# Kernel tuning notes

Measured on AMD Instinct MI355X. Metric: run time of the kernel, lower is better.

Reference implementation:

```python
import jax, jax.numpy as jnp
import numpy as np

B, N, F, C, K = 4, 8192, 128, 64, 16


def setup_inputs() -> dict:
    key = jax.random.key(0)
    ks = jax.random.split(key, 24)
    s = 0.05
    rn = lambda k, shape: (jax.random.normal(k, shape, jnp.float32) * s)
    return {
        "features": jax.random.normal(ks[0], (B, N, F), jnp.float32),
        "positions": jax.random.normal(ks[1], (B, N, 3), jnp.float32),
        "batch": jnp.repeat(jnp.arange(B, dtype=jnp.int32), N),
        "num_neighbors": K,
        # linear encoder (F -> C)
        "W_enc": rn(ks[2], (F, C)), "b_enc": jnp.zeros((C,), jnp.float32),
        # point-transformer q/k/v projections (C -> C)
        "Wq": rn(ks[3], (C, C)), "bq": jnp.zeros((C,), jnp.float32),
        "Wk": rn(ks[4], (C, C)), "bk": jnp.zeros((C,), jnp.float32),
        "Wv": rn(ks[5], (C, C)), "bv": jnp.zeros((C,), jnp.float32),
        # positional encoding MLP: 3 -> C -> C (ReLU)
        "Wp1": rn(ks[6], (3, C)), "bp1": jnp.zeros((C,), jnp.float32),
        "Wp2": rn(ks[7], (C, C)), "bp2": jnp.zeros((C,), jnp.float32),
        # attention MLP gamma: C -> C -> C (ReLU)
        "Wa1": rn(ks[8], (C, C)), "ba1": jnp.zeros((C,), jnp.float32),
        "Wa2": rn(ks[9], (C, C)), "ba2": jnp.zeros((C,), jnp.float32),
        # linear decoder (C -> F)
        "W_dec": rn(ks[10], (C, F)), "b_dec": jnp.zeros((F,), jnp.float32),
    }


def reference(features, positions, batch, num_neighbors,
              W_enc, b_enc, Wq, bq, Wk, bk, Wv, bv,
              Wp1, bp1, Wp2, bp2, Wa1, ba1, Wa2, ba2, W_dec, b_dec):
    # linear encode: [B,N,F] -> [B,N,C]
    x = features @ W_enc + b_enc
    q = x @ Wq + bq
    k = x @ Wk + bk
    v = x @ Wv + bv

    def per_cloud(pos, qi, ki, vi):
        # kNN via pairwise squared distances (self included, dist 0)
        sq = jnp.sum(pos * pos, axis=-1)                      # [N]
        d2 = sq[:, None] + sq[None, :] - 2.0 * (pos @ pos.T)  # [N,N]
        idx = jax.lax.top_k(-d2, num_neighbors)[1]            # [N,K]
        kj = ki[idx]                                          # [N,K,C] gather
        vj = vi[idx]                                          # [N,K,C]
        rel = pos[:, None, :] - pos[idx]                      # [N,K,3]
        # positional encoding delta = MLP(p_i - p_j)
        delta = jax.nn.relu(rel @ Wp1 + bp1) @ Wp2 + bp2      # [N,K,C]
        # vector attention: gamma(q_i - k_j + delta), softmax over K neighbors
        a = qi[:, None, :] - kj + delta
        a = jax.nn.relu(a @ Wa1 + ba1) @ Wa2 + ba2
        w = jax.nn.softmax(a, axis=1)                         # [N,K,C]
        return jnp.sum(w * (vj + delta), axis=1)              # [N,C]

    y = jax.vmap(per_cloud)(positions, q, k, v)               # [B,N,C]
    out = y @ W_dec + b_dec + features                        # decode + residual
    return (out, positions, batch)
```

## Files before the change

### kernel.cpp

```cpp
#include <hip/hip_runtime.h>
#include <hip/hip_bf16.h>

#define NPTS 32768
#define NPC  8192
#define KNN  16
#define CH   64
#define FDIM 128
#define NCELLS 4096
#define EMPTYKEY 0x7F7FFFFFu

typedef __bf16 bf16;
typedef __bf16 bf16x2 __attribute__((ext_vector_type(2)));
typedef __bf16 bf16x8 __attribute__((ext_vector_type(8)));
typedef float  f32x4  __attribute__((ext_vector_type(4)));

__device__ __forceinline__ unsigned spread4(unsigned v) {
    return (v & 1u) | ((v & 2u) << 2) | ((v & 4u) << 4) | ((v & 8u) << 6);
}

__global__ __launch_bounds__(1024) void k_sort(
    const float* __restrict__ pos, int* __restrict__ perm,
    int* __restrict__ invperm, float* __restrict__ posS)
{
    __shared__ unsigned hist[NCELLS];
    __shared__ unsigned short cellOf[NPC];
    __shared__ unsigned partial[1024];
    int cloud = blockIdx.x;
    int t = threadIdx.x;
    int cb = cloud * NPC;
    const float* pc = pos + (size_t)cb * 3;

    for (int i = t; i < NCELLS; i += 1024) hist[i] = 0;
    __syncthreads();

    for (int i = t; i < NPC; i += 1024) {
        float x = pc[i*3+0], y = pc[i*3+1], z = pc[i*3+2];
        int xi = (int)((x + 4.f) * 2.f); xi = xi < 0 ? 0 : (xi > 15 ? 15 : xi);
        int yi = (int)((y + 4.f) * 2.f); yi = yi < 0 ? 0 : (yi > 15 ? 15 : yi);
        int zi = (int)((z + 4.f) * 2.f); zi = zi < 0 ? 0 : (zi > 15 ? 15 : zi);
        unsigned m = (spread4((unsigned)xi) << 2) | (spread4((unsigned)yi) << 1) | spread4((unsigned)zi);
        cellOf[i] = (unsigned short)m;
        atomicAdd(&hist[m], 1u);
    }
    __syncthreads();

    unsigned s0 = hist[4*t+0], s1 = hist[4*t+1], s2 = hist[4*t+2], s3 = hist[4*t+3];
    unsigned tot = s0 + s1 + s2 + s3;
    partial[t] = tot;
    __syncthreads();
    for (int off = 1; off < 1024; off <<= 1) {
        unsigned v = (t >= off) ? partial[t - off] : 0u;
        __syncthreads();
        partial[t] += v;
        __syncthreads();
    }
    unsigned base = (t > 0) ? partial[t-1] : 0u;
    hist[4*t+0] = base;
    hist[4*t+1] = base + s0;
    hist[4*t+2] = base + s0 + s1;
    hist[4*t+3] = base + s0 + s1 + s2;
    __syncthreads();

    for (int i = t; i < NPC; i += 1024) {
        unsigned c = cellOf[i];
        unsigned s = atomicAdd(&hist[c], 1u);
        perm[cb + (int)s] = cb + i;
        invperm[cb + i] = cb + (int)s;
        posS[(size_t)(cb + (int)s)*3 + 0] = pc[i*3+0];
        posS[(size_t)(cb + (int)s)*3 + 1] = pc[i*3+1];
        posS[(size_t)(cb + (int)s)*3 + 2] = pc[i*3+2];
    }
}

__global__ __launch_bounds__(256) void k_encode(
    const float* __restrict__ feat, const int* __restrict__ perm,
    const float* __restrict__ Wenc, const float* __restrict__ benc,
    const float* __restrict__ Wq, const float* __restrict__ bq,
    const float* __restrict__ Wk, const float* __restrict__ bk,
    const float* __restrict__ Wv, const float* __restrict__ bv,
    bf16* __restrict__ qo, bf16* __restrict__ kvo)
{
    __shared__ float xs[4][CH];
    int t = threadIdx.x;
    int c = t & 63, pl = t >> 6;
    size_t pt = (size_t)blockIdx.x * 4 + pl;
    size_t orig = (size_t)perm[pt];
    const float* fr = feat + orig * FDIM;
    float acc = benc[c];
#pragma unroll 8
    for (int f4 = 0; f4 < 32; ++f4) {
        float4 fv = *reinterpret_cast<const float4*>(fr + f4 * 4);
        acc += fv.x * Wenc[(f4*4+0)*CH + c];
        acc += fv.y * Wenc[(f4*4+1)*CH + c];
        acc += fv.z * Wenc[(f4*4+2)*CH + c];
        acc += fv.w * Wenc[(f4*4+3)*CH + c];
    }
    xs[pl][c] = acc;
    __syncthreads();
    float aq = bq[c], ak = bk[c], av = bv[c];
#pragma unroll 4
    for (int m = 0; m < CH; ++m) {
        float xm = xs[pl][m];
        aq += xm * Wq[m*CH + c];
        ak += xm * Wk[m*CH + c];
        av += xm * Wv[m*CH + c];
    }
    qo[pt*CH + c] = (bf16)aq;
    bf16x2 kv2; kv2[0] = (bf16)ak; kv2[1] = (bf16)av;
    *reinterpret_cast<bf16x2*>(&kvo[pt*2*CH + 2*c]) = kv2;
}

__global__ __launch_bounds__(256, 4) void k_knn(
    const float* __restrict__ pos, unsigned* __restrict__ wsK)
{
    __shared__ float4 sp[1024];
    __shared__ unsigned sbuf[256 * 17];

    int t = threadIdx.x;
    int blk = blockIdx.x;
    int slice = blk & 7;
    int qg = (blk >> 3) & 31;
    int cloud = blk >> 8;
    const float* pc = pos + (size_t)cloud * NPC * 3;
    int jbase = slice << 10;

    {
        const float4* src = reinterpret_cast<const float4*>(pc + (size_t)jbase * 3);
        float4 a = src[t*3+0], b1 = src[t*3+1], c1 = src[t*3+2];
        sp[t*4+0] = make_float4(a.x,  a.y,  a.z,  0.f);
        sp[t*4+1] = make_float4(a.w,  b1.x, b1.y, 0.f);
        sp[t*4+2] = make_float4(b1.z, b1.w, c1.x, 0.f);
        sp[t*4+3] = make_float4(c1.y, c1.z, c1.w, 0.f);
    }
    __syncthreads();

    int qi = (qg << 8) + t;
    float myx = pc[qi*3+0], myy = pc[qi*3+1], myz = pc[qi*3+2];

    unsigned arr[16];
#pragma unroll
    for (int r = 0; r < 16; ++r) arr[r] = EMPTYKEY;
    float thrf = __uint_as_float(EMPTYKEY & 0xFFFFE000u);
    int cnt = 0;
    int base = t * 17;

    for (int g = 0; g < 1024; g += 4) {
        float d2v[4];
#pragma unroll
        for (int u = 0; u < 4; ++u) {
            float4 p = sp[g + u];
            float dx = myx - p.x, dy = myy - p.y, dz = myz - p.z;
            d2v[u] = dx*dx + dy*dy + dz*dz;
        }
        float m4 = fminf(fminf(d2v[0], d2v[1]), fminf(d2v[2], d2v[3]));
        if (__any(m4 <= thrf)) {
#pragma unroll
            for (int u = 0; u < 4; ++u) {
                if (d2v[u] <= thrf) {
                    sbuf[base + cnt] = (__float_as_uint(d2v[u]) & 0xFFFFE000u)
                                       | (unsigned)(jbase + g + u);
                    ++cnt;
                }
            }
            if (__any(cnt >= 13)) {
#pragma unroll
                for (int b = 0; b < 16; ++b) {
                    unsigned key = (b < cnt) ? sbuf[base + b] : EMPTYKEY;
                    if (key < arr[15]) {
#pragma unroll
                        for (int r = 0; r < 16; ++r) {
                            unsigned lo = min(key, arr[r]);
                            unsigned hi = max(key, arr[r]);
                            arr[r] = lo; key = hi;
                        }
                    }
                }
                cnt = 0;
                thrf = __uint_as_float(arr[15] & 0xFFFFE000u);
            }
        }
    }
#pragma unroll
    for (int b = 0; b < 16; ++b) {
        unsigned key = (b < cnt) ? sbuf[base + b] : EMPTYKEY;
        if (key < arr[15]) {
#pragma unroll
            for (int r = 0; r < 16; ++r) {
                unsigned lo = min(key, arr[r]);
                unsigned hi = max(key, arr[r]);
                arr[r] = lo; key = hi;
            }
        }
    }
    size_t gq = (size_t)cloud * NPC + qi;
#pragma unroll
    for (int r = 0; r < 16; ++r) wsK[(size_t)(slice*16 + r)*NPTS + gq] = arr[r];
}

__global__ __launch_bounds__(64) void k_merge(
    const unsigned* __restrict__ wsK, const int* __restrict__ invperm,
    int* __restrict__ idxout,
    const float* __restrict__ Wp2, const float* __restrict__ Wa1,
    const float* __restrict__ Wa2, bf16* __restrict__ wpk)
{
    __shared__ unsigned kk[64][137];
    int t = threadIdx.x;
    size_t q = (size_t)blockIdx.x * 64 + t;
    int cb = (int)((q >> 13) << 13);
#pragma unroll
    for (int l = 0; l < 8; ++l) {
#pragma unroll
        for (int r = 0; r < 16; ++r)
            kk[t][l*17 + r] = wsK[(size_t)(l*16 + r)*NPTS + q];
        kk[t][l*17 + 16] = 0xFFFFFFFFu;
    }

    int sq = invperm[q];
    unsigned h0=0,h1=0,h2=0,h3=0,h4=0,h5=0,h6=0,h7=0;
    int* o = idxout + (size_t)sq * KNN;
    for (int r = 0; r < KNN; ++r) {
        unsigned best = 0xFFFFFFFFu; int bl = 0; unsigned k;
        k = kk[t][0*17 + h0]; if (k < best) { best = k; bl = 0; }
        k = kk[t][1*17 + h1]; if (k < best) { best = k; bl = 1; }
        k = kk[t][2*17 + h2]; if (k < best) { best = k; bl = 2; }
        k = kk[t][3*17 + h3]; if (k < best) { best = k; bl = 3; }
        k = kk[t][4*17 + h4]; if (k < best) { best = k; bl = 4; }
        k = kk[t][5*17 + h5]; if (k < best) { best = k; bl = 5; }
        k = kk[t][6*17 + h6]; if (k < best) { best = k; bl = 6; }
        k = kk[t][7*17 + h7]; if (k < best) { best = k; bl = 7; }
        o[r] = invperm[cb + (int)(best & 0x1FFFu)] - cb;
        h0 += (bl == 0); h1 += (bl == 1); h2 += (bl == 2); h3 += (bl == 3);
        h4 += (bl == 4); h5 += (bl == 5); h6 += (bl == 6); h7 += (bl == 7);
    }

    if (blockIdx.x == 0) {
        int lane = t;
        int mlane = lane & 15, kgrp = lane >> 4;
        const float* Ws[3] = {Wp2, Wa1, Wa2};
        bf16x8* ow = reinterpret_cast<bf16x8*>(wpk);
        for (int gmm = 0; gmm < 3; ++gmm) {
#pragma unroll
            for (int nt = 0; nt < 4; ++nt) {
#pragma unroll
                for (int kt = 0; kt < 2; ++kt) {
                    bf16x8 v;
#pragma unroll
                    for (int j = 0; j < 8; ++j)
                        v[j] = (bf16)Ws[gmm][(kt*32 + kgrp*8 + j)*CH + nt*16 + mlane];
                    ow[(gmm*8 + nt*2 + kt)*64 + lane] = v;
                }
            }
        }
    }
}

__device__ __forceinline__ void wave_gemm(
    const bf16* At, f32x4 (&acc)[4][4], const bf16x8* __restrict__ wpk,
    int w, int lane)
{
    int kgrp = lane >> 4;
    bf16x8 wf[4][2];
#pragma unroll
    for (int nt = 0; nt < 4; ++nt)
#pragma unroll
        for (int kt = 0; kt < 2; ++kt)
            wf[nt][kt] = wpk[(nt*2 + kt)*64 + lane];
#pragma unroll
    for (int mt = 0; mt < 4; ++mt) {
        int row = w*64 + mt*16 + (lane & 15);
        const bf16* rb = At + row*CH;
        int sw = row & 7;
        bf16x8 a0 = *reinterpret_cast<const bf16x8*>(rb + ((kgrp     ^ sw) * 8));
        bf16x8 a1 = *reinterpret_cast<const bf16x8*>(rb + (((4+kgrp) ^ sw) * 8));
#pragma unroll
        for (int nt = 0; nt < 4; ++nt) {
            acc[mt][nt] = __builtin_amdgcn_mfma_f32_16x16x32_bf16(a0, wf[nt][0], acc[mt][nt], 0, 0, 0);
            acc[mt][nt] = __builtin_amdgcn_mfma_f32_16x16x32_bf16(a1, wf[nt][1], acc[mt][nt], 0, 0, 0);
        }
    }
}

__global__ __launch_bounds__(128, 3) void k_attn(
    const float* __restrict__ pos, const int* __restrict__ nidx,
    const bf16* __restrict__ qg, const bf16* __restrict__ kvg,
    const float* __restrict__ Wp1, const float* __restrict__ bp1,
    const float* __restrict__ bp2, const float* __restrict__ ba1,
    const float* __restrict__ ba2, const bf16* __restrict__ wpkg,
    float* __restrict__ yout)
{
    __shared__ bf16 At[128 * CH];

    int t = threadIdx.x;
    int w = t >> 6, lane = t & 63;
    int mlane = lane & 15, kgrp = lane >> 4;
    int blk0 = blockIdx.x;
    int blk = ((blk0 & 7) << 9) | (blk0 >> 3);
    size_t p0 = (size_t)blk * 8;
    size_t cbase = (p0 >> 13) << 13;
    const bf16x2* kv2 = reinterpret_cast<const bf16x2*>(kvg);
    const bf16x8* wpk = reinterpret_cast<const bf16x8*>(wpkg);

    {
        int p = t >> 4, j = t & 15;
        size_t gp = p0 + p;
        int nbr = nidx[gp*KNN + j];
        size_t gn = cbase + (size_t)nbr;
        float rx = pos[gp*3+0] - pos[gn*3+0];
        float ry = pos[gp*3+1] - pos[gn*3+1];
        float rz = pos[gp*3+2] - pos[gn*3+2];
        float h[CH];
#pragma unroll
        for (int c4 = 0; c4 < 16; ++c4) {
            float4 w0 = *reinterpret_cast<const float4*>(Wp1 + 0*CH + c4*4);
            float4 w1 = *reinterpret_cast<const float4*>(Wp1 + 1*CH + c4*4);
            float4 w2 = *reinterpret_cast<const float4*>(Wp1 + 2*CH + c4*4);
            float4 bb = *reinterpret_cast<const float4*>(bp1 + c4*4);
            h[c4*4+0] = fmaxf(rx*w0.x + ry*w1.x + rz*w2.x + bb.x, 0.f);
            h[c4*4+1] = fmaxf(rx*w0.y + ry*w1.y + rz*w2.y + bb.y, 0.f);
            h[c4*4+2] = fmaxf(rx*w0.z + ry*w1.z + rz*w2.z + bb.z, 0.f);
            h[c4*4+3] = fmaxf(rx*w0.w + ry*w1.w + rz*w2.w + bb.w, 0.f);
        }
#pragma unroll
        for (int ch = 0; ch < 8; ++ch) {
            bf16x8 v;
#pragma unroll
            for (int e = 0; e < 8; ++e) v[e] = (bf16)h[ch*8 + e];
            *reinterpret_cast<bf16x8*>(&At[t*CH + (ch ^ (t & 7)) * 8]) = v;
        }
    }

    f32x4 acc[4][4];

#pragma unroll
    for (int nt = 0; nt < 4; ++nt) {
        float b = bp2[nt*16 + mlane];
#pragma unroll
        for (int mt = 0; mt < 4; ++mt) { acc[mt][nt][0]=b; acc[mt][nt][1]=b; acc[mt][nt][2]=b; acc[mt][nt][3]=b; }
    }
    wave_gemm(At, acc, wpk, w, lane);

    bf16x2 vdp[4][4][2];
#pragma unroll
    for (int mt = 0; mt < 4; ++mt) {
        size_t gp = p0 + (size_t)(w*4 + mt);
        int nb[4];
#pragma unroll
        for (int reg = 0; reg < 4; ++reg)
            nb[reg] = nidx[gp*KNN + kgrp*4 + reg];
#pragma unroll
        for (int nt = 0; nt < 4; ++nt) {
            int c = nt*16 + mlane;
            float qv = (float)qg[gp*CH + c];
            float vdf[4];
#pragma unroll
            for (int reg = 0; reg < 4; ++reg) {
                float dlt = acc[mt][nt][reg];
                size_t gr = cbase + (size_t)nb[reg];
                bf16x2 kvp = kv2[gr*CH + c];
                float kvf = (float)kvp[0];
                float vv  = (float)kvp[1];
                int row = w*64 + mt*16 + kgrp*4 + reg;
                int off = row*CH + (((c >> 3) ^ (row & 7)) * 8) + (c & 7);
                At[off] = (bf16)(qv - kvf + dlt);
                vdf[reg] = vv + dlt;
            }
            bf16x2 lo2; lo2[0] = (bf16)vdf[0]; lo2[1] = (bf16)vdf[1];
            bf16x2 hi2; hi2[0] = (bf16)vdf[2]; hi2[1] = (bf16)vdf[3];
            vdp[mt][nt][0] = lo2;
            vdp[mt][nt][1] = hi2;
        }
    }

#pragma unroll
    for (int nt = 0; nt < 4; ++nt) {
        float b = ba1[nt*16 + mlane];
#pragma unroll
        for (int mt = 0; mt < 4; ++mt) { acc[mt][nt][0]=b; acc[mt][nt][1]=b; acc[mt][nt][2]=b; acc[mt][nt][3]=b; }
    }
    wave_gemm(At, acc, wpk + 512, w, lane);
#pragma unroll
    for (int mt = 0; mt < 4; ++mt) {
#pragma unroll
        for (int nt = 0; nt < 4; ++nt) {
            int c = nt*16 + mlane;
#pragma unroll
            for (int reg = 0; reg < 4; ++reg) {
                int row = w*64 + mt*16 + kgrp*4 + reg;
                int off = row*CH + (((c >> 3) ^ (row & 7)) * 8) + (c & 7);
                At[off] = (bf16)fmaxf(acc[mt][nt][reg], 0.f);
            }
        }
    }

#pragma unroll
    for (int nt = 0; nt < 4; ++nt) {
        float b = ba2[nt*16 + mlane];
#pragma unroll
        for (int mt = 0; mt < 4; ++mt) { acc[mt][nt][0]=b; acc[mt][nt][1]=b; acc[mt][nt][2]=b; acc[mt][nt][3]=b; }
    }
    wave_gemm(At, acc, wpk + 1024, w, lane);

#pragma unroll
    for (int mt = 0; mt < 4; ++mt) {
        size_t gp = p0 + (size_t)(w*4 + mt);
#pragma unroll
        for (int nt = 0; nt < 4; ++nt) {
            int c = nt*16 + mlane;
            float m = fmaxf(fmaxf(acc[mt][nt][0], acc[mt][nt][1]),
                            fmaxf(acc[mt][nt][2], acc[mt][nt][3]));
            m = fmaxf(m, __shfl_xor(m, 16));
            m = fmaxf(m, __shfl_xor(m, 32));
            float e[4], s = 0.f;
#pragma unroll
            for (int reg = 0; reg < 4; ++reg) { e[reg] = __expf(acc[mt][nt][reg] - m); s += e[reg]; }
            s += __shfl_xor(s, 16);
            s += __shfl_xor(s, 32);
            float num = 0.f;
            num += e[0] * (float)vdp[mt][nt][0][0];
            num += e[1] * (float)vdp[mt][nt][0][1];
            num += e[2] * (float)vdp[mt][nt][1][0];
            num += e[3] * (float)vdp[mt][nt][1][1];
            num += __shfl_xor(num, 16);
            num += __shfl_xor(num, 32);
            if (kgrp == 0) yout[gp*CH + c] = num / s;
        }
    }
}

__global__ __launch_bounds__(256) void k_decode(
    const float* __restrict__ y, const int* __restrict__ invperm,
    const float* __restrict__ Wd, const float* __restrict__ bd,
    const float* __restrict__ feat, const float* __restrict__ pos,
    const int* __restrict__ batch, float* __restrict__ out)
{
    int t = threadIdx.x;
    int f = t & 127, pl = t >> 7;
    size_t pt = (size_t)blockIdx.x * 2 + pl;
    const float* yr = y + (size_t)invperm[pt]*CH;
    float acc = bd[f] + feat[pt*FDIM + f];
#pragma unroll
    for (int c4 = 0; c4 < 16; ++c4) {
        float4 yv = *reinterpret_cast<const float4*>(yr + c4*4);
        acc += yv.x * Wd[(c4*4+0)*FDIM + f];
        acc += yv.y * Wd[(c4*4+1)*FDIM + f];
        acc += yv.z * Wd[(c4*4+2)*FDIM + f];
        acc += yv.w * Wd[(c4*4+3)*FDIM + f];
    }
    out[pt*FDIM + f] = acc;

    int i = blockIdx.x * 256 + t;
    if (i < NPTS*3) out[(size_t)NPTS*FDIM + i] = pos[i];
    if (i < NPTS)   out[(size_t)NPTS*FDIM + NPTS*3 + i] = (float)batch[i];
}

extern "C" void kernel_launch(void* const* d_in, const int* in_sizes, int n_in,
                              void* d_out, int out_size, void* d_ws, size_t ws_size,
                              hipStream_t stream)
{
    const float* feat  = (const float*)d_in[0];
    const float* pos   = (const float*)d_in[1];
    const int*   batch = (const int*)d_in[2];
    const float* Wenc  = (const float*)d_in[4];
    const float* benc  = (const float*)d_in[5];
    const float* Wq = (const float*)d_in[6];   const float* bq = (const float*)d_in[7];
    const float* Wk = (const float*)d_in[8];   const float* bk = (const float*)d_in[9];
    const float* Wv = (const float*)d_in[10];  const float* bv = (const float*)d_in[11];
    const float* Wp1= (const float*)d_in[12];  const float* bp1= (const float*)d_in[13];
    const float* Wp2= (const float*)d_in[14];  const float* bp2= (const float*)d_in[15];
    const float* Wa1= (const float*)d_in[16];  const float* ba1= (const float*)d_in[17];
    const float* Wa2= (const float*)d_in[18];  const float* ba2= (const float*)d_in[19];
    const float* Wd = (const float*)d_in[20];  const float* bd = (const float*)d_in[21];
    float* out = (float*)d_out;

    char* W = (char*)d_ws;
    int*      idx = (int*)W;
    unsigned* wsK = (unsigned*)(W + (size_t)NPTS*KNN*4);
    bf16* qb  = (bf16*)wsK;
    bf16* kvb = qb + (size_t)NPTS*CH;
    float* yb = (float*)(W + (size_t)NPTS*KNN*4 + (size_t)NPTS*KNN*8*4);
    bf16*  wpk = (bf16*)(yb + (size_t)NPTS*CH);
    int*   perm    = (int*)((char*)wpk + 32768);
    int*   invperm = perm + NPTS;
    float* posS    = (float*)(invperm + NPTS);

    k_sort<<<4, 1024, 0, stream>>>(pos, perm, invperm, posS);
    k_knn<<<1024, 256, 0, stream>>>(pos, wsK);
    k_merge<<<NPTS/64, 64, 0, stream>>>(wsK, invperm, idx, Wp2, Wa1, Wa2, wpk);

    k_encode<<<NPTS/4, 256, 0, stream>>>(feat, perm, Wenc, benc, Wq, bq, Wk, bk, Wv, bv, qb, kvb);

    k_attn<<<NPTS/8, 128, 0, stream>>>(posS, idx, qb, kvb,
                                       Wp1, bp1, bp2, ba1, ba2, wpk, yb);

    k_decode<<<NPTS/2, 256, 0, stream>>>(yb, invperm, Wd, bd, feat, pos, batch, out);
}
```

Measured before the change: 476.4 us.

## Compute kNN distances with bf16 split-precision MFMA instead of scalar FMA

The brute-force kNN distance loop now runs on the matrix cores via mfma_f32_16x16x32_bf16. Coordinates are split into hi/lo bf16 parts to keep roughly fp32 accuracy, and a norm term is folded in. The work is repartitioned so each lane handles one query against a quarter of each 16-candidate tile, with candidates staged into LDS in chunks. Occupancy is lowered to 3 blocks per CU to fit the larger shared tile. The bf16 split could misorder near-tied neighbors, and per-lane candidate insertion stays scalar.

```diff
diff --git a/kernel.cpp b/kernel.cpp
--- a/kernel.cpp
+++ b/kernel.cpp
@@ -110,32 +110,34 @@
     *reinterpret_cast<bf16x2*>(&kvo[pt*2*CH + 2*c]) = kv2;
 }
 
-__global__ __launch_bounds__(256, 4) void k_knn(
+__global__ __launch_bounds__(256, 3) void k_knn(
     const float* __restrict__ pos, unsigned* __restrict__ wsK)
 {
-    __shared__ float4 sp[1024];
+    __shared__ bf16 Atile[1024 * 16];
     __shared__ unsigned sbuf[256 * 17];
 
     int t = threadIdx.x;
     int blk = blockIdx.x;
-    int slice = blk & 7;
-    int qg = (blk >> 3) & 31;
     int cloud = blk >> 8;
+    int half  = blk & 1;
+    int qg    = (blk >> 1) & 127;
     const float* pc = pos + (size_t)cloud * NPC * 3;
-    int jbase = slice << 10;
-
-    {
-        const float4* src = reinterpret_cast<const float4*>(pc + (size_t)jbase * 3);
-        float4 a = src[t*3+0], b1 = src[t*3+1], c1 = src[t*3+2];
-        sp[t*4+0] = make_float4(a.x,  a.y,  a.z,  0.f);
-        sp[t*4+1] = make_float4(a.w,  b1.x, b1.y, 0.f);
-        sp[t*4+2] = make_float4(b1.z, b1.w, c1.x, 0.f);
-        sp[t*4+3] = make_float4(c1.y, c1.z, c1.w, 0.f);
-    }
-    __syncthreads();
-
-    int qi = (qg << 8) + t;
-    float myx = pc[qi*3+0], myy = pc[qi*3+1], myz = pc[qi*3+2];
+
+    int w = t >> 6, lane = t & 63;
+    int col = lane & 15, kgrp = lane >> 4;
+
+    int q = qg*64 + w*16 + col;
+    float qx = pc[q*3+0], qy = pc[q*3+1], qz = pc[q*3+2];
+    float qq = fmaf(qx, qx, fmaf(qy, qy, qz*qz));
+    float nx = -qx, ny = -qy, nz = -qz;
+    bf16 nhx = (bf16)nx; bf16 nlx = (bf16)(nx - (float)nhx);
+    bf16 nhy = (bf16)ny; bf16 nly = (bf16)(ny - (float)nhy);
+    bf16 nhz = (bf16)nz; bf16 nlz = (bf16)(nz - (float)nhz);
+    bf16 Z = (bf16)0.f, ONE = (bf16)1.f;
+    bf16x8 bfrag;
+    if (kgrp == 0)      bfrag = (bf16x8){nhx,nhy,nhz,nhx,nhy,nhz,nlx,nly};
+    else if (kgrp == 1) bfrag = (bf16x8){nlz,ONE,ONE,nlx,nly,nlz,Z,Z};
+    else                bfrag = (bf16x8){Z,Z,Z,Z,Z,Z,Z,Z};
 
     unsigned arr[16];
 #pragma unroll
@@ -144,21 +146,38 @@
     int cnt = 0;
     int base = t * 17;
 
-    for (int g = 0; g < 1024; g += 4) {
-        float d2v[4];
-#pragma unroll
-        for (int u = 0; u < 4; ++u) {
-            float4 p = sp[g + u];
-            float dx = myx - p.x, dy = myy - p.y, dz = myz - p.z;
-            d2v[u] = dx*dx + dy*dy + dz*dz;
-        }
-        float m4 = fminf(fminf(d2v[0], d2v[1]), fminf(d2v[2], d2v[3]));
-        if (__any(m4 <= thrf)) {
-#pragma unroll
-            for (int u = 0; u < 4; ++u) {
-                if (d2v[u] <= thrf) {
-                    sbuf[base + cnt] = (__float_as_uint(d2v[u]) & 0xFFFFE000u)
-                                       | (unsigned)(jbase + g + u);
+    for (int chunk = 0; chunk < 4; ++chunk) {
+        __syncthreads();
+#pragma unroll
+        for (int i = 0; i < 4; ++i) {
+            int lc = i*256 + t;
+            int cand = half*4096 + chunk*1024 + lc;
+            float px = pc[cand*3+0], py = pc[cand*3+1], pz = pc[cand*3+2];
+            float wv = 0.5f * fmaf(px, px, fmaf(py, py, pz*pz));
+            bf16 phx = (bf16)px; bf16 plx = (bf16)(px - (float)phx);
+            bf16 phy = (bf16)py; bf16 ply = (bf16)(py - (float)phy);
+            bf16 phz = (bf16)pz; bf16 plz = (bf16)(pz - (float)phz);
+            bf16 wh  = (bf16)wv; bf16 wl  = (bf16)(wv - (float)wh);
+            bf16x8 lo = (bf16x8){phx,phy,phz,plx,ply,plz,phx,phy};
+            bf16x8 hi = (bf16x8){phz,wh,wl,plx,ply,plz,Z,Z};
+            int off = (lc >> 4)*256 + (lc & 15)*16;
+            *reinterpret_cast<bf16x8*>(&Atile[off])     = lo;
+            *reinterpret_cast<bf16x8*>(&Atile[off + 8]) = hi;
+        }
+        __syncthreads();
+
+        int cb0 = half*4096 + chunk*1024 + kgrp*4;
+        for (int tile = 0; tile < 64; ++tile) {
+            int aoff = tile*256 + col*16 + (kgrp & 1)*8;
+            bf16x8 a = *reinterpret_cast<const bf16x8*>(&Atile[aoff]);
+            f32x4 acc = {0.f, 0.f, 0.f, 0.f};
+            acc = __builtin_amdgcn_mfma_f32_16x16x32_bf16(a, bfrag, acc, 0, 0, 0);
+#pragma unroll
+            for (int reg = 0; reg < 4; ++reg) {
+                float d2 = fmaxf(fmaf(2.f, acc[reg], qq), 0.f);
+                if (d2 <= thrf) {
+                    sbuf[base + cnt] = (__float_as_uint(d2) & 0xFFFFE000u)
+                                       | (unsigned)(cb0 + tile*16 + reg);
                     ++cnt;
                 }
             }
@@ -169,9 +188,9 @@
                     if (key < arr[15]) {
 #pragma unroll
                         for (int r = 0; r < 16; ++r) {
-                            unsigned lo = min(key, arr[r]);
-                            unsigned hi = max(key, arr[r]);
-                            arr[r] = lo; key = hi;
+                            unsigned klo = min(key, arr[r]);
+                            unsigned khi = max(key, arr[r]);
+                            arr[r] = klo; key = khi;
                         }
                     }
                 }
@@ -186,15 +205,16 @@
         if (key < arr[15]) {
 #pragma unroll
             for (int r = 0; r < 16; ++r) {
-                unsigned lo = min(key, arr[r]);
-                unsigned hi = max(key, arr[r]);
-                arr[r] = lo; key = hi;
+                unsigned klo = min(key, arr[r]);
+                unsigned khi = max(key, arr[r]);
+                arr[r] = klo; key = khi;
             }
         }
     }
-    size_t gq = (size_t)cloud * NPC + qi;
-#pragma unroll
-    for (int r = 0; r < 16; ++r) wsK[(size_t)(slice*16 + r)*NPTS + gq] = arr[r];
+    size_t gq = (size_t)cloud * NPC + q;
+    int sub = half*4 + kgrp;
+#pragma unroll
+    for (int r = 0; r < 16; ++r) wsK[(size_t)(sub*16 + r)*NPTS + gq] = arr[r];
 }
 
 __global__ __launch_bounds__(64) void k_merge(
```

Result: no change. 485.8 us (+2.0%).

## Replace brute-force sliced kNN with uniform-grid shell search over sorted cells

Applied to the files above, without the earlier changes.

The sort kernel now also writes per-cell start offsets, and a new grid kNN kernel searches expanding Chebyshev shells of cells around each query. It stops once the lower bound on distance to the next shell exceeds the current 16th-best. This replaces the brute-force 8-slice scan over all points plus the merge kernel, cutting distance evaluations from O(N) to near-local counts. Weight packing moves to its own tiny kernel. The risks are warp divergence from uneven cell occupancy, uncoalesced global reads of the sorted positions, and small launch sizes (64-thread blocks).

```diff
diff --git a/kernel.cpp b/kernel.cpp
--- a/kernel.cpp
+++ b/kernel.cpp
@@ -20,7 +20,8 @@
 
 __global__ __launch_bounds__(1024) void k_sort(
     const float* __restrict__ pos, int* __restrict__ perm,
-    int* __restrict__ invperm, float* __restrict__ posS)
+    int* __restrict__ invperm, float* __restrict__ posS,
+    int* __restrict__ cellStartG)
 {
     __shared__ unsigned hist[NCELLS];
     __shared__ unsigned short cellOf[NPC];
@@ -59,6 +60,12 @@
     hist[4*t+1] = base + s0;
     hist[4*t+2] = base + s0 + s1;
     hist[4*t+3] = base + s0 + s1 + s2;
+    int* csg = cellStartG + cloud * (NCELLS + 1);
+    csg[4*t+0] = (int)hist[4*t+0];
+    csg[4*t+1] = (int)hist[4*t+1];
+    csg[4*t+2] = (int)hist[4*t+2];
+    csg[4*t+3] = (int)hist[4*t+3];
+    if (t == 0) csg[NCELLS] = NPC;
     __syncthreads();
 
     for (int i = t; i < NPC; i += 1024) {
@@ -69,6 +76,29 @@
         posS[(size_t)(cb + (int)s)*3 + 0] = pc[i*3+0];
         posS[(size_t)(cb + (int)s)*3 + 1] = pc[i*3+1];
         posS[(size_t)(cb + (int)s)*3 + 2] = pc[i*3+2];
+    }
+}
+
+__global__ __launch_bounds__(64) void k_pack(
+    const float* __restrict__ Wp2, const float* __restrict__ Wa1,
+    const float* __restrict__ Wa2, bf16* __restrict__ wpk)
+{
+    int lane = threadIdx.x;
+    int mlane = lane & 15, kgrp = lane >> 4;
+    const float* Ws[3] = {Wp2, Wa1, Wa2};
+    bf16x8* o = reinterpret_cast<bf16x8*>(wpk);
+    for (int gmm = 0; gmm < 3; ++gmm) {
+#pragma unroll
+        for (int nt = 0; nt < 4; ++nt) {
+#pragma unroll
+            for (int kt = 0; kt < 2; ++kt) {
+                bf16x8 v;
+#pragma unroll
+                for (int j = 0; j < 8; ++j)
+                    v[j] = (bf16)Ws[gmm][(kt*32 + kgrp*8 + j)*CH + nt*16 + mlane];
+                o[(gmm*8 + nt*2 + kt)*64 + lane] = v;
+            }
+        }
     }
 }
 
@@ -110,148 +140,90 @@
     *reinterpret_cast<bf16x2*>(&kvo[pt*2*CH + 2*c]) = kv2;
 }
 
-__global__ __launch_bounds__(256, 4) void k_knn(
-    const float* __restrict__ pos, unsigned* __restrict__ wsK)
-{
-    __shared__ float4 sp[1024];
-    __shared__ unsigned sbuf[256 * 17];
-
+__global__ __launch_bounds__(64) void k_gknn(
+    const float* __restrict__ posS, const int* __restrict__ cellStartG,
+    const int* __restrict__ perm, const int* __restrict__ invperm,
+    int* __restrict__ idxout)
+{
+    __shared__ unsigned sp4[16];
     int t = threadIdx.x;
-    int blk = blockIdx.x;
-    int slice = blk & 7;
-    int qg = (blk >> 3) & 31;
-    int cloud = blk >> 8;
-    const float* pc = pos + (size_t)cloud * NPC * 3;
-    int jbase = slice << 10;
-
-    {
-        const float4* src = reinterpret_cast<const float4*>(pc + (size_t)jbase * 3);
-        float4 a = src[t*3+0], b1 = src[t*3+1], c1 = src[t*3+2];
-        sp[t*4+0] = make_float4(a.x,  a.y,  a.z,  0.f);
-        sp[t*4+1] = make_float4(a.w,  b1.x, b1.y, 0.f);
-        sp[t*4+2] = make_float4(b1.z, b1.w, c1.x, 0.f);
-        sp[t*4+3] = make_float4(c1.y, c1.z, c1.w, 0.f);
-    }
-    __syncthreads();
-
-    int qi = (qg << 8) + t;
-    float myx = pc[qi*3+0], myy = pc[qi*3+1], myz = pc[qi*3+2];
+    if (t < 16) sp4[t] = spread4((unsigned)t);
+    __syncthreads();
+
+    int sq = blockIdx.x * 64 + t;
+    int cloud = sq >> 13;
+    int cb = cloud << 13;
+    int lq = sq & (NPC - 1);
+    const float* pc = posS + (size_t)cb * 3;
+    const int* cs = cellStartG + cloud * (NCELLS + 1);
+    const int* pm = perm + cb;
+    const int* iv = invperm + cb;
+
+    float x = pc[lq*3+0], y = pc[lq*3+1], z = pc[lq*3+2];
+    int cx = (int)((x + 4.f) * 2.f); cx = cx < 0 ? 0 : (cx > 15 ? 15 : cx);
+    int cy = (int)((y + 4.f) * 2.f); cy = cy < 0 ? 0 : (cy > 15 ? 15 : cy);
+    int cz = (int)((z + 4.f) * 2.f); cz = cz < 0 ? 0 : (cz > 15 ? 15 : cz);
+    float fx = x - ((float)cx * 0.5f - 4.f);
+    float fy = y - ((float)cy * 0.5f - 4.f);
+    float fz = z - ((float)cz * 0.5f - 4.f);
+    float m = fminf(fminf(fminf(fx, 0.5f - fx), fminf(fy, 0.5f - fy)),
+                    fminf(fz, 0.5f - fz));
 
     unsigned arr[16];
 #pragma unroll
     for (int r = 0; r < 16; ++r) arr[r] = EMPTYKEY;
     float thrf = __uint_as_float(EMPTYKEY & 0xFFFFE000u);
-    int cnt = 0;
-    int base = t * 17;
-
-    for (int g = 0; g < 1024; g += 4) {
-        float d2v[4];
-#pragma unroll
-        for (int u = 0; u < 4; ++u) {
-            float4 p = sp[g + u];
-            float dx = myx - p.x, dy = myy - p.y, dz = myz - p.z;
-            d2v[u] = dx*dx + dy*dy + dz*dz;
-        }
-        float m4 = fminf(fminf(d2v[0], d2v[1]), fminf(d2v[2], d2v[3]));
-        if (__any(m4 <= thrf)) {
-#pragma unroll
-            for (int u = 0; u < 4; ++u) {
-                if (d2v[u] <= thrf) {
-                    sbuf[base + cnt] = (__float_as_uint(d2v[u]) & 0xFFFFE000u)
-                                       | (unsigned)(jbase + g + u);
-                    ++cnt;
-                }
-            }
-            if (__any(cnt >= 13)) {
-#pragma unroll
-                for (int b = 0; b < 16; ++b) {
-                    unsigned key = (b < cnt) ? sbuf[base + b] : EMPTYKEY;
-                    if (key < arr[15]) {
-#pragma unroll
-                        for (int r = 0; r < 16; ++r) {
-                            unsigned lo = min(key, arr[r]);
-                            unsigned hi = max(key, arr[r]);
-                            arr[r] = lo; key = hi;
+
+    for (int s = 0; s <= 15; ++s) {
+        float lb = fmaxf((float)(s - 1) * 0.5f + m, 0.f);
+        bool active = (lb * lb <= thrf);
+        if (!__any(active)) break;
+        if (active) {
+            int x0 = cx - s < 0 ? 0 : cx - s, x1 = cx + s > 15 ? 15 : cx + s;
+            int y0 = cy - s < 0 ? 0 : cy - s, y1 = cy + s > 15 ? 15 : cy + s;
+            int z0 = cz - s < 0 ? 0 : cz - s, z1 = cz + s > 15 ? 15 : cz + s;
+            for (int ix = x0; ix <= x1; ++ix) {
+                int adx = ix > cx ? ix - cx : cx - ix;
+                unsigned mx = sp4[ix] << 2;
+                for (int iy = y0; iy <= y1; ++iy) {
+                    int ady = iy > cy ? iy - cy : cy - iy;
+                    int am = adx > ady ? adx : ady;
+                    unsigned mxy = mx | (sp4[iy] << 1);
+                    for (int iz = z0; iz <= z1; ++iz) {
+                        int adz = iz > cz ? iz - cz : cz - iz;
+                        int ch = am > adz ? am : adz;
+                        if (ch != s) continue;
+                        unsigned mc = mxy | sp4[iz];
+                        int b0 = cs[mc], b1 = cs[mc + 1];
+                        for (int j = b0; j < b1; ++j) {
+                            float dx = x - pc[j*3+0];
+                            float dy = y - pc[j*3+1];
+                            float dz = z - pc[j*3+2];
+                            float d2 = dx*dx + dy*dy + dz*dz;
+                            if (d2 <= thrf) {
+                                unsigned key = (__float_as_uint(d2) & 0xFFFFE000u)
+                                             | (unsigned)(pm[j] - cb);
+                                if (key < arr[15]) {
+#pragma unroll
+                                    for (int r = 0; r < 16; ++r) {
+                                        unsigned klo = min(key, arr[r]);
+                                        unsigned khi = max(key, arr[r]);
+                                        arr[r] = klo; key = khi;
+                                    }
+                                    thrf = __uint_as_float(arr[15] & 0xFFFFE000u);
+                                }
+                            }
                         }
                     }
                 }
-                cnt = 0;
-                thrf = __uint_as_float(arr[15] & 0xFFFFE000u);
             }
         }
     }
-#pragma unroll
-    for (int b = 0; b < 16; ++b) {
-        unsigned key = (b < cnt) ? sbuf[base + b] : EMPTYKEY;
-        if (key < arr[15]) {
-#pragma unroll
-            for (int r = 0; r < 16; ++r) {
-                unsigned lo = min(key, arr[r]);
-                unsigned hi = max(key, arr[r]);
-                arr[r] = lo; key = hi;
-            }
-        }
-    }
-    size_t gq = (size_t)cloud * NPC + qi;
-#pragma unroll
-    for (int r = 0; r < 16; ++r) wsK[(size_t)(slice*16 + r)*NPTS + gq] = arr[r];
-}
-
-__global__ __launch_bounds__(64) void k_merge(
-    const unsigned* __restrict__ wsK, const int* __restrict__ invperm,
-    int* __restrict__ idxout,
-    const float* __restrict__ Wp2, const float* __restrict__ Wa1,
-    const float* __restrict__ Wa2, bf16* __restrict__ wpk)
-{
-    __shared__ unsigned kk[64][137];
-    int t = threadIdx.x;
-    size_t q = (size_t)blockIdx.x * 64 + t;
-    int cb = (int)((q >> 13) << 13);
-#pragma unroll
-    for (int l = 0; l < 8; ++l) {
-#pragma unroll
-        for (int r = 0; r < 16; ++r)
-            kk[t][l*17 + r] = wsK[(size_t)(l*16 + r)*NPTS + q];
-        kk[t][l*17 + 16] = 0xFFFFFFFFu;
-    }
-
-    int sq = invperm[q];
-    unsigned h0=0,h1=0,h2=0,h3=0,h4=0,h5=0,h6=0,h7=0;
+
     int* o = idxout + (size_t)sq * KNN;
-    for (int r = 0; r < KNN; ++r) {
-        unsigned best = 0xFFFFFFFFu; int bl = 0; unsigned k;
-        k = kk[t][0*17 + h0]; if (k < best) { best = k; bl = 0; }
-        k = kk[t][1*17 + h1]; if (k < best) { best = k; bl = 1; }
-        k = kk[t][2*17 + h2]; if (k < best) { best = k; bl = 2; }
-        k = kk[t][3*17 + h3]; if (k < best) { best = k; bl = 3; }
-        k = kk[t][4*17 + h4]; if (k < best) { best = k; bl = 4; }
-        k = kk[t][5*17 + h5]; if (k < best) { best = k; bl = 5; }
-        k = kk[t][6*17 + h6]; if (k < best) { best = k; bl = 6; }
-        k = kk[t][7*17 + h7]; if (k < best) { best = k; bl = 7; }
-        o[r] = invperm[cb + (int)(best & 0x1FFFu)] - cb;
-        h0 += (bl == 0); h1 += (bl == 1); h2 += (bl == 2); h3 += (bl == 3);
-        h4 += (bl == 4); h5 += (bl == 5); h6 += (bl == 6); h7 += (bl == 7);
-    }
-
-    if (blockIdx.x == 0) {
-        int lane = t;
-        int mlane = lane & 15, kgrp = lane >> 4;
-        const float* Ws[3] = {Wp2, Wa1, Wa2};
-        bf16x8* ow = reinterpret_cast<bf16x8*>(wpk);
-        for (int gmm = 0; gmm < 3; ++gmm) {
-#pragma unroll
-            for (int nt = 0; nt < 4; ++nt) {
-#pragma unroll
-                for (int kt = 0; kt < 2; ++kt) {
-                    bf16x8 v;
-#pragma unroll
-                    for (int j = 0; j < 8; ++j)
-                        v[j] = (bf16)Ws[gmm][(kt*32 + kgrp*8 + j)*CH + nt*16 + mlane];
-                    ow[(gmm*8 + nt*2 + kt)*64 + lane] = v;
-                }
-            }
-        }
-    }
+#pragma unroll
+    for (int r = 0; r < 16; ++r)
+        o[r] = iv[(int)(arr[r] & 0x1FFFu)] - cb;
 }
 
 __device__ __forceinline__ void wave_gemm(
@@ -473,19 +445,19 @@
     float* out = (float*)d_out;
 
     char* W = (char*)d_ws;
-    int*      idx = (int*)W;
-    unsigned* wsK = (unsigned*)(W + (size_t)NPTS*KNN*4);
-    bf16* qb  = (bf16*)wsK;
-    bf16* kvb = qb + (size_t)NPTS*CH;
-    float* yb = (float*)(W + (size_t)NPTS*KNN*4 + (size_t)NPTS*KNN*8*4);
-    bf16*  wpk = (bf16*)(yb + (size_t)NPTS*CH);
-    int*   perm    = (int*)((char*)wpk + 32768);
-    int*   invperm = perm + NPTS;
-    float* posS    = (float*)(invperm + NPTS);
-
-    k_sort<<<4, 1024, 0, stream>>>(pos, perm, invperm, posS);
-    k_knn<<<1024, 256, 0, stream>>>(pos, wsK);
-    k_merge<<<NPTS/64, 64, 0, stream>>>(wsK, invperm, idx, Wp2, Wa1, Wa2, wpk);
+    int*  idx = (int*)W;                                   W += (size_t)NPTS*KNN*4;
+    bf16* qb  = (bf16*)W;                                  W += (size_t)NPTS*CH*2;
+    bf16* kvb = (bf16*)W;                                  W += (size_t)NPTS*2*CH*2;
+    float* yb = (float*)W;                                 W += (size_t)NPTS*CH*4;
+    bf16*  wpk = (bf16*)W;                                 W += 32768;
+    int*   perm    = (int*)W;                              W += (size_t)NPTS*4;
+    int*   invperm = (int*)W;                              W += (size_t)NPTS*4;
+    float* posS    = (float*)W;                            W += (size_t)NPTS*3*4;
+    int*   cellStart = (int*)W;
+
+    k_sort<<<4, 1024, 0, stream>>>(pos, perm, invperm, posS, cellStart);
+    k_pack<<<1, 64, 0, stream>>>(Wp2, Wa1, Wa2, wpk);
+    k_gknn<<<NPTS/64, 64, 0, stream>>>(posS, cellStart, perm, invperm, idx);
 
     k_encode<<<NPTS/4, 256, 0, stream>>>(feat, perm, Wenc, benc, Wq, bq, Wk, bk, Wv, bv, qb, kvb);
 
```

Result: slower. 1.052 ms (+120.8%).

## Replace brute-force kNN with uniform-grid cell search over sorted points

Applied to the files above, without the earlier changes.

The sort kernel now bins points into an 8x8x8 grid and exports per-cell start offsets. A new kNN kernel walks expanding shells of cells around each wave's bounding box of query cells, visiting only candidate points in nearby cells and stopping once the shell lower bound exceeds the current 16th-best threshold. This replaces the brute-force scan over all 8192 points per cloud. Work is split across 8 cell-parity slices for the merge kernel, and the attention kernel's occupancy hint is raised. Global memory reads of candidates are uncoalesced and wave divergence depends on the point distribution.

```diff
diff --git a/kernel.cpp b/kernel.cpp
--- a/kernel.cpp
+++ b/kernel.cpp
@@ -6,7 +6,8 @@
 #define KNN  16
 #define CH   64
 #define FDIM 128
-#define NCELLS 4096
+#define NC3  512
+#define CSS  513
 #define EMPTYKEY 0x7F7FFFFFu
 
 typedef __bf16 bf16;
@@ -14,51 +15,53 @@
 typedef __bf16 bf16x8 __attribute__((ext_vector_type(8)));
 typedef float  f32x4  __attribute__((ext_vector_type(4)));
 
-__device__ __forceinline__ unsigned spread4(unsigned v) {
-    return (v & 1u) | ((v & 2u) << 2) | ((v & 4u) << 4) | ((v & 8u) << 6);
+__device__ __forceinline__ unsigned s3(unsigned v) {
+    return (v & 1u) | ((v & 2u) << 2) | ((v & 4u) << 4);
 }
 
 __global__ __launch_bounds__(1024) void k_sort(
     const float* __restrict__ pos, int* __restrict__ perm,
-    int* __restrict__ invperm, float* __restrict__ posS)
-{
-    __shared__ unsigned hist[NCELLS];
+    int* __restrict__ invperm, float* __restrict__ posS,
+    int* __restrict__ cellStartG)
+{
+    __shared__ unsigned hist[NC3];
     __shared__ unsigned short cellOf[NPC];
-    __shared__ unsigned partial[1024];
+    __shared__ unsigned scan[NC3];
     int cloud = blockIdx.x;
     int t = threadIdx.x;
     int cb = cloud * NPC;
     const float* pc = pos + (size_t)cb * 3;
 
-    for (int i = t; i < NCELLS; i += 1024) hist[i] = 0;
+    if (t < NC3) hist[t] = 0;
     __syncthreads();
 
     for (int i = t; i < NPC; i += 1024) {
         float x = pc[i*3+0], y = pc[i*3+1], z = pc[i*3+2];
-        int xi = (int)((x + 4.f) * 2.f); xi = xi < 0 ? 0 : (xi > 15 ? 15 : xi);
-        int yi = (int)((y + 4.f) * 2.f); yi = yi < 0 ? 0 : (yi > 15 ? 15 : yi);
-        int zi = (int)((z + 4.f) * 2.f); zi = zi < 0 ? 0 : (zi > 15 ? 15 : zi);
-        unsigned m = (spread4((unsigned)xi) << 2) | (spread4((unsigned)yi) << 1) | spread4((unsigned)zi);
+        int xi = (int)(x + 4.f); xi = xi < 0 ? 0 : (xi > 7 ? 7 : xi);
+        int yi = (int)(y + 4.f); yi = yi < 0 ? 0 : (yi > 7 ? 7 : yi);
+        int zi = (int)(z + 4.f); zi = zi < 0 ? 0 : (zi > 7 ? 7 : zi);
+        unsigned m = s3((unsigned)xi) | (s3((unsigned)yi) << 1) | (s3((unsigned)zi) << 2);
         cellOf[i] = (unsigned short)m;
         atomicAdd(&hist[m], 1u);
     }
     __syncthreads();
 
-    unsigned s0 = hist[4*t+0], s1 = hist[4*t+1], s2 = hist[4*t+2], s3 = hist[4*t+3];
-    unsigned tot = s0 + s1 + s2 + s3;
-    partial[t] = tot;
+    if (t < NC3) scan[t] = hist[t];
     __syncthreads();
-    for (int off = 1; off < 1024; off <<= 1) {
-        unsigned v = (t >= off) ? partial[t - off] : 0u;
+    for (int off = 1; off < NC3; off <<= 1) {
+        unsigned v = 0;
+        if (t < NC3 && t >= off) v = scan[t - off];
         __syncthreads();
-        partial[t] += v;
+        if (t < NC3) scan[t] += v;
         __syncthreads();
     }
-    unsigned base = (t > 0) ? partial[t-1] : 0u;
-    hist[4*t+0] = base;
-    hist[4*t+1] = base + s0;
-    hist[4*t+2] = base + s0 + s1;
-    hist[4*t+3] = base + s0 + s1 + s2;
+    int* csg = cellStartG + cloud * CSS;
+    if (t < NC3) {
+        unsigned st = scan[t] - hist[t];
+        hist[t] = st;
+        csg[t] = (int)st;
+    }
+    if (t == 0) csg[NC3] = NPC;
     __syncthreads();
 
     for (int i = t; i < NPC; i += 1024) {
@@ -69,6 +72,166 @@
         posS[(size_t)(cb + (int)s)*3 + 0] = pc[i*3+0];
         posS[(size_t)(cb + (int)s)*3 + 1] = pc[i*3+1];
         posS[(size_t)(cb + (int)s)*3 + 2] = pc[i*3+2];
+    }
+}
+
+__global__ __launch_bounds__(256) void k_cknn(
+    const float* __restrict__ posS, const int* __restrict__ cellStartG,
+    const int* __restrict__ perm, unsigned* __restrict__ wsK)
+{
+    __shared__ unsigned sbuf[256 * 12];
+    int t = threadIdx.x;
+    int w = t >> 6, lane = t & 63;
+    int blk = blockIdx.x;
+    int qgroup = blk >> 1;
+    int split  = ((blk & 1) << 2) | w;
+    int sq = qgroup * 64 + lane;
+    int cloud = sq >> 13;
+    int cb = cloud << 13;
+    int lq = sq & (NPC - 1);
+    const float* pc = posS + (size_t)cb * 3;
+    const int* cs = cellStartG + cloud * CSS;
+    const int* pm = perm + cb;
+
+    float x = pc[lq*3+0], y = pc[lq*3+1], z = pc[lq*3+2];
+    int cx = (int)(x + 4.f); cx = cx < 0 ? 0 : (cx > 7 ? 7 : cx);
+    int cy = (int)(y + 4.f); cy = cy < 0 ? 0 : (cy > 7 ? 7 : cy);
+    int cz = (int)(z + 4.f); cz = cz < 0 ? 0 : (cz > 7 ? 7 : cz);
+
+    int bx0 = cx, bx1 = cx, by0 = cy, by1 = cy, bz0 = cz, bz1 = cz;
+#pragma unroll
+    for (int o = 1; o < 64; o <<= 1) {
+        bx0 = min(bx0, __shfl_xor(bx0, o)); bx1 = max(bx1, __shfl_xor(bx1, o));
+        by0 = min(by0, __shfl_xor(by0, o)); by1 = max(by1, __shfl_xor(by1, o));
+        bz0 = min(bz0, __shfl_xor(bz0, o)); bz1 = max(bz1, __shfl_xor(bz1, o));
+    }
+
+    unsigned arr[16];
+#pragma unroll
+    for (int r = 0; r < 16; ++r) arr[r] = EMPTYKEY;
+    float thrf = __uint_as_float(EMPTYKEY & 0xFFFFE000u);
+    int cnt = 0;
+    int base = t * 12;
+
+    int px0 = 1, px1 = 0, py0 = 1, py1 = 0, pz0 = 1, pz1 = 0;
+    for (int s = 0; s <= 8; ++s) {
+        float lb = fmaxf((float)(s - 1), 0.f);
+        if (!__any(lb * lb <= thrf * 1.002f)) break;
+        int ex0 = max(bx0 - s, 0), ex1 = min(bx1 + s, 7);
+        int ey0 = max(by0 - s, 0), ey1 = min(by1 + s, 7);
+        int ez0 = max(bz0 - s, 0), ez1 = min(bz1 + s, 7);
+        for (int ix = ex0; ix <= ex1; ++ix) {
+            for (int iy = ey0; iy <= ey1; ++iy) {
+                for (int iz = ez0; iz <= ez1; ++iz) {
+                    if (ix >= px0 && ix <= px1 && iy >= py0 && iy <= py1 &&
+                        iz >= pz0 && iz <= pz1) continue;
+                    if (((ix + 2*iy + 4*iz) & 7) != split) continue;
+                    unsigned mc = s3((unsigned)ix) | (s3((unsigned)iy) << 1)
+                                | (s3((unsigned)iz) << 2);
+                    int j0 = cs[mc], j1 = cs[mc + 1];
+                    for (int j = j0; j < j1; ++j) {
+                        float dx = x - pc[j*3+0];
+                        float dy = y - pc[j*3+1];
+                        float dz = z - pc[j*3+2];
+                        float d2 = dx*dx + dy*dy + dz*dz;
+                        if (d2 <= thrf) {
+                            int oj = pm[j] - cb;
+                            sbuf[base + cnt] = (__float_as_uint(d2) & 0xFFFFE000u)
+                                             | (unsigned)oj;
+                            ++cnt;
+                        }
+                        if (__any(cnt >= 9)) {
+#pragma unroll
+                            for (int b = 0; b < 12; ++b) {
+                                unsigned key = (b < cnt) ? sbuf[base + b] : EMPTYKEY;
+                                if (key < arr[15]) {
+#pragma unroll
+                                    for (int r = 0; r < 16; ++r) {
+                                        unsigned klo = min(key, arr[r]);
+                                        unsigned khi = max(key, arr[r]);
+                                        arr[r] = klo; key = khi;
+                                    }
+                                }
+                            }
+                            cnt = 0;
+                            thrf = __uint_as_float(arr[15] & 0xFFFFE000u);
+                        }
+                    }
+                }
+            }
+        }
+        px0 = ex0; px1 = ex1; py0 = ey0; py1 = ey1; pz0 = ez0; pz1 = ez1;
+    }
+#pragma unroll
+    for (int b = 0; b < 12; ++b) {
+        unsigned key = (b < cnt) ? sbuf[base + b] : EMPTYKEY;
+        if (key < arr[15]) {
+#pragma unroll
+            for (int r = 0; r < 16; ++r) {
+                unsigned klo = min(key, arr[r]);
+                unsigned khi = max(key, arr[r]);
+                arr[r] = klo; key = khi;
+            }
+        }
+    }
+#pragma unroll
+    for (int r = 0; r < 16; ++r) wsK[(size_t)(split*16 + r)*NPTS + sq] = arr[r];
+}
+
+__global__ __launch_bounds__(64) void k_merge(
+    const unsigned* __restrict__ wsK, const int* __restrict__ invperm,
+    int* __restrict__ idxout,
+    const float* __restrict__ Wp2, const float* __restrict__ Wa1,
+    const float* __restrict__ Wa2, bf16* __restrict__ wpk)
+{
+    __shared__ unsigned kk[64][137];
+    int t = threadIdx.x;
+    size_t q = (size_t)blockIdx.x * 64 + t;
+    int cb = (int)((q >> 13) << 13);
+#pragma unroll
+    for (int l = 0; l < 8; ++l) {
+#pragma unroll
+        for (int r = 0; r < 16; ++r)
+            kk[t][l*17 + r] = wsK[(size_t)(l*16 + r)*NPTS + q];
+        kk[t][l*17 + 16] = 0xFFFFFFFFu;
+    }
+
+    const int* iv = invperm + cb;
+    unsigned h0=0,h1=0,h2=0,h3=0,h4=0,h5=0,h6=0,h7=0;
+    int* o = idxout + q * KNN;
+    for (int r = 0; r < KNN; ++r) {
+        unsigned best = 0xFFFFFFFFu; int bl = 0; unsigned k;
+        k = kk[t][0*17 + h0]; if (k < best) { best = k; bl = 0; }
+        k = kk[t][1*17 + h1]; if (k < best) { best = k; bl = 1; }
+        k = kk[t][2*17 + h2]; if (k < best) { best = k; bl = 2; }
+        k = kk[t][3*17 + h3]; if (k < best) { best = k; bl = 3; }
+        k = kk[t][4*17 + h4]; if (k < best) { best = k; bl = 4; }
+        k = kk[t][5*17 + h5]; if (k < best) { best = k; bl = 5; }
+        k = kk[t][6*17 + h6]; if (k < best) { best = k; bl = 6; }
+        k = kk[t][7*17 + h7]; if (k < best) { best = k; bl = 7; }
+        o[r] = iv[(int)(best & 0x1FFFu)] - cb;
+        h0 += (bl == 0); h1 += (bl == 1); h2 += (bl == 2); h3 += (bl == 3);
+        h4 += (bl == 4); h5 += (bl == 5); h6 += (bl == 6); h7 += (bl == 7);
+    }
+
+    if (blockIdx.x == 0) {
+        int lane = t;
+        int mlane = lane & 15, kgrp = lane >> 4;
+        const float* Ws[3] = {Wp2, Wa1, Wa2};
+        bf16x8* ow = reinterpret_cast<bf16x8*>(wpk);
+        for (int gmm = 0; gmm < 3; ++gmm) {
+#pragma unroll
+            for (int nt = 0; nt < 4; ++nt) {
+#pragma unroll
+                for (int kt = 0; kt < 2; ++kt) {
+                    bf16x8 v;
+#pragma unroll
+                    for (int j = 0; j < 8; ++j)
+                        v[j] = (bf16)Ws[gmm][(kt*32 + kgrp*8 + j)*CH + nt*16 + mlane];
+                    ow[(gmm*8 + nt*2 + kt)*64 + lane] = v;
+                }
+            }
+        }
     }
 }
 
@@ -110,150 +273,6 @@
     *reinterpret_cast<bf16x2*>(&kvo[pt*2*CH + 2*c]) = kv2;
 }
 
-__global__ __launch_bounds__(256, 4) void k_knn(
-    const float* __restrict__ pos, unsigned* __restrict__ wsK)
-{
-    __shared__ float4 sp[1024];
-    __shared__ unsigned sbuf[256 * 17];
-
-    int t = threadIdx.x;
-    int blk = blockIdx.x;
-    int slice = blk & 7;
-    int qg = (blk >> 3) & 31;
-    int cloud = blk >> 8;
-    const float* pc = pos + (size_t)cloud * NPC * 3;
-    int jbase = slice << 10;
-
-    {
-        const float4* src = reinterpret_cast<const float4*>(pc + (size_t)jbase * 3);
-        float4 a = src[t*3+0], b1 = src[t*3+1], c1 = src[t*3+2];
-        sp[t*4+0] = make_float4(a.x,  a.y,  a.z,  0.f);
-        sp[t*4+1] = make_float4(a.w,  b1.x, b1.y, 0.f);
-        sp[t*4+2] = make_float4(b1.z, b1.w, c1.x, 0.f);
-        sp[t*4+3] = make_float4(c1.y, c1.z, c1.w, 0.f);
-    }
-    __syncthreads();
-
-    int qi = (qg << 8) + t;
-    float myx = pc[qi*3+0], myy = pc[qi*3+1], myz = pc[qi*3+2];
-
-    unsigned arr[16];
-#pragma unroll
-    for (int r = 0; r < 16; ++r) arr[r] = EMPTYKEY;
-    float thrf = __uint_as_float(EMPTYKEY & 0xFFFFE000u);
-    int cnt = 0;
-    int base = t * 17;
-
-    for (int g = 0; g < 1024; g += 4) {
-        float d2v[4];
-#pragma unroll
-        for (int u = 0; u < 4; ++u) {
-            float4 p = sp[g + u];
-            float dx = myx - p.x, dy = myy - p.y, dz = myz - p.z;
-            d2v[u] = dx*dx + dy*dy + dz*dz;
-        }
-        float m4 = fminf(fminf(d2v[0], d2v[1]), fminf(d2v[2], d2v[3]));
-        if (__any(m4 <= thrf)) {
-#pragma unroll
-            for (int u = 0; u < 4; ++u) {
-                if (d2v[u] <= thrf) {
-                    sbuf[base + cnt] = (__float_as_uint(d2v[u]) & 0xFFFFE000u)
-                                       | (unsigned)(jbase + g + u);
-                    ++cnt;
-                }
-            }
-            if (__any(cnt >= 13)) {
-#pragma unroll
-                for (int b = 0; b < 16; ++b) {
-                    unsigned key = (b < cnt) ? sbuf[base + b] : EMPTYKEY;
-                    if (key < arr[15]) {
-#pragma unroll
-                        for (int r = 0; r < 16; ++r) {
-                            unsigned lo = min(key, arr[r]);
-                            unsigned hi = max(key, arr[r]);
-                            arr[r] = lo; key = hi;
-                        }
-                    }
-                }
-                cnt = 0;
-                thrf = __uint_as_float(arr[15] & 0xFFFFE000u);
-            }
-        }
-    }
-#pragma unroll
-    for (int b = 0; b < 16; ++b) {
-        unsigned key = (b < cnt) ? sbuf[base + b] : EMPTYKEY;
-        if (key < arr[15]) {
-#pragma unroll
-            for (int r = 0; r < 16; ++r) {
-                unsigned lo = min(key, arr[r]);
-                unsigned hi = max(key, arr[r]);
-                arr[r] = lo; key = hi;
-            }
-        }
-    }
-    size_t gq = (size_t)cloud * NPC + qi;
-#pragma unroll
-    for (int r = 0; r < 16; ++r) wsK[(size_t)(slice*16 + r)*NPTS + gq] = arr[r];
-}
-
-__global__ __launch_bounds__(64) void k_merge(
-    const unsigned* __restrict__ wsK, const int* __restrict__ invperm,
-    int* __restrict__ idxout,
-    const float* __restrict__ Wp2, const float* __restrict__ Wa1,
-    const float* __restrict__ Wa2, bf16* __restrict__ wpk)
-{
-    __shared__ unsigned kk[64][137];
-    int t = threadIdx.x;
-    size_t q = (size_t)blockIdx.x * 64 + t;
-    int cb = (int)((q >> 13) << 13);
-#pragma unroll
-    for (int l = 0; l < 8; ++l) {
-#pragma unroll
-        for (int r = 0; r < 16; ++r)
-            kk[t][l*17 + r] = wsK[(size_t)(l*16 + r)*NPTS + q];
-        kk[t][l*17 + 16] = 0xFFFFFFFFu;
-    }
-
-    int sq = invperm[q];
-    unsigned h0=0,h1=0,h2=0,h3=0,h4=0,h5=0,h6=0,h7=0;
-    int* o = idxout + (size_t)sq * KNN;
-    for (int r = 0; r < KNN; ++r) {
-        unsigned best = 0xFFFFFFFFu; int bl = 0; unsigned k;
-        k = kk[t][0*17 + h0]; if (k < best) { best = k; bl = 0; }
-        k = kk[t][1*17 + h1]; if (k < best) { best = k; bl = 1; }
-        k = kk[t][2*17 + h2]; if (k < best) { best = k; bl = 2; }
-        k = kk[t][3*17 + h3]; if (k < best) { best = k; bl = 3; }
-        k = kk[t][4*17 + h4]; if (k < best) { best = k; bl = 4; }
-        k = kk[t][5*17 + h5]; if (k < best) { best = k; bl = 5; }
-        k = kk[t][6*17 + h6]; if (k < best) { best = k; bl = 6; }
-        k = kk[t][7*17 + h7]; if (k < best) { best = k; bl = 7; }
-        o[r] = invperm[cb + (int)(best & 0x1FFFu)] - cb;
-        h0 += (bl == 0); h1 += (bl == 1); h2 += (bl == 2); h3 += (bl == 3);
-        h4 += (bl == 4); h5 += (bl == 5); h6 += (bl == 6); h7 += (bl == 7);
-    }
-
-    if (blockIdx.x == 0) {
-        int lane = t;
-        int mlane = lane & 15, kgrp = lane >> 4;
-        const float* Ws[3] = {Wp2, Wa1, Wa2};
-        bf16x8* ow = reinterpret_cast<bf16x8*>(wpk);
-        for (int gmm = 0; gmm < 3; ++gmm) {
-#pragma unroll
-            for (int nt = 0; nt < 4; ++nt) {
-#pragma unroll
-                for (int kt = 0; kt < 2; ++kt) {
-                    bf16x8 v;
-#pragma unroll
-                    for (int j = 0; j < 8; ++j)
-                        v[j] = (bf16)Ws[gmm][(kt*32 + kgrp*8 + j)*CH + nt*16 + mlane];
-                    ow[(gmm*8 + nt*2 + kt)*64 + lane] = v;
-                }
-            }
-        }
-    }
-}
-
 __device__ __forceinline__ void wave_gemm(
     const bf16* At, f32x4 (&acc)[4][4], const bf16x8* __restrict__ wpk,
     int w, int lane)
@@ -280,7 +299,7 @@
     }
 }
 
-__global__ __launch_bounds__(128, 3) void k_attn(
+__global__ __launch_bounds__(128, 6) void k_attn(
     const float* __restrict__ pos, const int* __restrict__ nidx,
     const bf16* __restrict__ qg, const bf16* __restrict__ kvg,
     const float* __restrict__ Wp1, const float* __restrict__ bp1,
@@ -473,18 +492,19 @@
     float* out = (float*)d_out;
 
     char* W = (char*)d_ws;
-    int*      idx = (int*)W;
-    unsigned* wsK = (unsigned*)(W + (size_t)NPTS*KNN*4);
+    int*      idx = (int*)W;                               W += (size_t)NPTS*KNN*4;
+    unsigned* wsK = (unsigned*)W;
     bf16* qb  = (bf16*)wsK;
-    bf16* kvb = qb + (size_t)NPTS*CH;
-    float* yb = (float*)(W + (size_t)NPTS*KNN*4 + (size_t)NPTS*KNN*8*4);
-    bf16*  wpk = (bf16*)(yb + (size_t)NPTS*CH);
-    int*   perm    = (int*)((char*)wpk + 32768);
-    int*   invperm = perm + NPTS;
-    float* posS    = (float*)(invperm + NPTS);
-
-    k_sort<<<4, 1024, 0, stream>>>(pos, perm, invperm, posS);
-    k_knn<<<1024, 256, 0, stream>>>(pos, wsK);
+    bf16* kvb = qb + (size_t)NPTS*CH;                      W += (size_t)NPTS*KNN*8*4;
+    float* yb = (float*)W;                                 W += (size_t)NPTS*CH*4;
+    bf16*  wpk = (bf16*)W;                                 W += 32768;
+    int*   perm    = (int*)W;                              W += (size_t)NPTS*4;
+    int*   invperm = (int*)W;                              W += (size_t)NPTS*4;
+    float* posS    = (float*)W;                            W += (size_t)NPTS*3*4;
+    int*   cellStart = (int*)W;
+
+    k_sort<<<4, 1024, 0, stream>>>(pos, perm, invperm, posS, cellStart);
+    k_cknn<<<1024, 256, 0, stream>>>(posS, cellStart, perm, wsK);
     k_merge<<<NPTS/64, 64, 0, stream>>>(wsK, invperm, idx, Wp2, Wa1, Wa2, wpk);
 
     k_encode<<<NPTS/4, 256, 0, stream>>>(feat, perm, Wenc, benc, Wq, bq, Wk, bk, Wv, bv, qb, kvb);
```

After: 704.4 us. 47.9% more time.
